# Kernel optimization log

Hardware: AMD Instinct MI355X
Metric: run time of the kernel (lower is better)

The kernel has to match this reference:

```python
import jax, jax.numpy as jnp
import numpy as np

N_EMB = 1024
EMB_DIM = 256
BETA = 0.25


def setup_inputs() -> dict:
    key = jax.random.key(0)
    k1, k2 = jax.random.split(key)
    z = jax.random.normal(k1, (32, EMB_DIM, 32, 32), dtype=jnp.float32)
    init = 1.0 / N_EMB
    emb = jax.random.uniform(k2, (N_EMB, EMB_DIM), dtype=jnp.float32,
                             minval=-init, maxval=init)
    return {"z": z, "emb": emb}


def reference(z, emb):
    # z: [B, C, H, W] -> [B, H, W, C]
    zc = jnp.transpose(z, (0, 2, 3, 1))
    z_flat = zc.reshape(-1, EMB_DIM)  # [N, D]

    # squared L2 distances: ||z||^2 + ||e||^2 - 2 z.e^T  -> [N, K]
    distances = (jnp.sum(z_flat ** 2, axis=1, keepdims=True)
                 + jnp.sum(emb ** 2, axis=1)
                 - 2.0 * (z_flat @ emb.T))
    nearest_idx = jnp.argmin(distances, axis=1)           # [N]
    nearest = jax.nn.one_hot(nearest_idx, N_EMB, dtype=jnp.float32)  # [N, K]

    # direct gather == one-hot matmul, same math
    zq = emb[nearest_idx].reshape(zc.shape)               # [B, H, W, C]

    loss = (jnp.mean((jax.lax.stop_gradient(zq) - zc) ** 2)
            + BETA * jnp.mean((zq - jax.lax.stop_gradient(zc)) ** 2))

    # straight-through estimator
    zq_st = zc + jax.lax.stop_gradient(zq - zc)

    e_mean = jnp.mean(nearest, axis=0)                    # [K]
    perplexity = jnp.exp(-jnp.sum(e_mean * jnp.log(e_mean + 1e-10)))

    zq_out = jnp.transpose(zq_st, (0, 3, 1, 2))           # back to NCHW
    return zq_out, loss, perplexity, nearest, nearest_idx[:, None]
```

## Files before the change

kernel.cpp:

```cpp
#include <hip/hip_runtime.h>

#define N_EMB  1024
#define EMB_D  256
#define HW     1024

#define OUT_ZQ      0
#define OUT_LOSS    8388608
#define OUT_PERP    8388609
#define OUT_NEAREST 8388610
#define OUT_IDX     41943042

#define WS_HIST   0
#define WS_ESQ    4096
#define WS_LOSSP  8192
#define WS_EH     12288
#define WS_TOTAL  536576

typedef unsigned long long ull;
typedef _Float16 half8 __attribute__((ext_vector_type(8)));
typedef float f32x4 __attribute__((ext_vector_type(4)));
typedef ull ull2 __attribute__((ext_vector_type(2)));

#define L_A     0
#define L_B     32768
#define L_ESQ   49152
#define L_ZSQ   53248
#define L_WIN   53504
#define L_RED   53760
#define L_TOT   55808

__device__ __forceinline__ void gload16(const void* g, void* l) {
    __builtin_amdgcn_global_load_lds(
        (const __attribute__((address_space(1))) unsigned int*)g,
        (__attribute__((address_space(3))) unsigned int*)l, 16, 0, 0);
}

__device__ __forceinline__ float pairwise8_combine(const float r[8]) {
    return __fadd_rn(__fadd_rn(__fadd_rn(r[0], r[1]), __fadd_rn(r[2], r[3])),
                     __fadd_rn(__fadd_rn(r[4], r[5]), __fadd_rn(r[6], r[7])));
}

__global__ void split_e(const float* __restrict__ emb, _Float16* __restrict__ eh) {
    int c = blockIdx.x;
    int k = threadIdx.x;
    eh[c * EMB_D + k] = (_Float16)emb[c * EMB_D + k];
}

__global__ void esq_kernel(const float* __restrict__ emb, float* __restrict__ esq,
                           int* __restrict__ hist) {
    int c = blockIdx.x * 256 + threadIdx.x;
    const float* p = emb + (size_t)c * EMB_D;
    float tot[2];
    #pragma unroll
    for (int h = 0; h < 2; ++h) {
        float r[8];
        #pragma unroll
        for (int i = 0; i < 8; ++i) {
            float x = p[h * 128 + i];
            r[i] = __fmul_rn(x, x);
        }
        for (int k = 8; k < 128; k += 8) {
            #pragma unroll
            for (int i = 0; i < 8; ++i) {
                float x = p[h * 128 + k + i];
                r[i] = __fadd_rn(r[i], __fmul_rn(x, x));
            }
        }
        tot[h] = pairwise8_combine(r);
    }
    esq[c] = __fadd_rn(tot[0], tot[1]);
    hist[c] = 0;
}

__global__ __launch_bounds__(256) void fused_vq(
        const float* __restrict__ z, const float* __restrict__ emb,
        const _Float16* __restrict__ eh, const float* __restrict__ esq,
        float* __restrict__ out, int* __restrict__ hist,
        double* __restrict__ lossp) {
    __shared__ __align__(16) char lds[L_TOT];
    int t = threadIdx.x, bid = blockIdx.x;
    int b = bid >> 4, hw0 = (bid & 15) << 6;
    int lane = t & 63, wave = t >> 6;
    int wm = wave >> 1, wn = wave & 1;
    int l15 = lane & 15, lq = lane >> 4;

    if (t >= 128) {
        int i = t - 128;
        #pragma unroll
        for (int q = 0; q < 8; ++q)
            *(float*)(lds + L_ESQ + (q * 128 + i) * 4) = esq[q * 128 + i];
    } else {
        int nl = t & 63, h = (t >> 6) & 1;
        const float* zp = z + ((size_t)b << 18) + hw0 + nl;
        int kb = h << 7;
        int abase = L_A + nl * 512;
        int sw = (nl & 7) << 4;
        float r[8];
        {   half8 hv;
            #pragma unroll
            for (int e = 0; e < 8; ++e) {
                float x = zp[(size_t)(kb + e) << 10];
                hv[e] = (_Float16)x;
                r[e] = __fmul_rn(x, x);
            }
            *(half8*)(lds + abase + (((kb << 1)) ^ sw)) = hv;
        }
        for (int c8 = 1; c8 < 16; ++c8) {
            half8 hv;
            #pragma unroll
            for (int e = 0; e < 8; ++e) {
                float x = zp[(size_t)(kb + c8 * 8 + e) << 10];
                hv[e] = (_Float16)x;
                r[e] = __fadd_rn(r[e], __fmul_rn(x, x));
            }
            *(half8*)(lds + abase + (((kb << 1) + c8 * 16) ^ sw)) = hv;
        }
        *(float*)(lds + L_RED + (h * 64 + nl) * 4) = pairwise8_combine(r);
    }
    __syncthreads();
    if (t < 64) {
        float t0 = *(float*)(lds + L_RED + t * 4);
        float t1 = *(float*)(lds + L_RED + 256 + t * 4);
        *(float*)(lds + L_ZSQ + t * 4) = __fadd_rn(t0, t1);
    }
    __syncthreads();

    int aoffs[2][2], boffs[4][2];
    #pragma unroll
    for (int i = 0; i < 2; ++i) {
        int r = wm * 32 + i * 16 + l15;
        #pragma unroll
        for (int kc = 0; kc < 2; ++kc)
            aoffs[i][kc] = L_A + r * 512 + ((kc * 64 + lq * 16) ^ ((r & 7) << 4));
    }
    #pragma unroll
    for (int j = 0; j < 4; ++j) {
        int c = wn * 64 + j * 16 + l15;
        #pragma unroll
        for (int kc = 0; kc < 2; ++kc)
            boffs[j][kc] = L_B + c * 128 + ((kc * 64 + lq * 16) ^ ((c & 7) << 4));
    }
    int bsrc[4], bdst[4];
    #pragma unroll
    for (int is = 0; is < 4; ++is) {
        int o = is * 4096 + t * 16;
        int col = o >> 7;
        int K = (o & 127) ^ ((col & 7) << 4);
        bsrc[is] = col * 256 + (K >> 1);
        bdst[is] = L_B + o;
    }
    float zs[8];
    #pragma unroll
    for (int s = 0; s < 8; ++s) {
        int row = wm * 32 + (s >> 2) * 16 + lq * 4 + (s & 3);
        zs[s] = *(const float*)(lds + L_ZSQ + row * 4);
    }
    ull k1[8], k2[8];
    #pragma unroll
    for (int s = 0; s < 8; ++s) { k1[s] = ~0ULL; k2[s] = ~0ULL; }

    for (int cbt = 0; cbt < 8; ++cbt) {
        f32x4 acc[2][4];
        #pragma unroll
        for (int i = 0; i < 2; ++i)
            #pragma unroll
            for (int j = 0; j < 4; ++j) acc[i][j] = (f32x4){0.f, 0.f, 0.f, 0.f};

        for (int kt = 0; kt < 4; ++kt) {
            __syncthreads();
            #pragma unroll
            for (int is = 0; is < 4; ++is)
                gload16(eh + cbt * 32768 + kt * 64 + bsrc[is], lds + bdst[is]);
            __syncthreads();

            half8 a[2][2], bb[4][2];
            #pragma unroll
            for (int i = 0; i < 2; ++i) {
                a[i][0] = *(const half8*)(lds + aoffs[i][0] + kt * 128);
                a[i][1] = *(const half8*)(lds + aoffs[i][1] + kt * 128);
            }
            #pragma unroll
            for (int j = 0; j < 4; ++j) {
                bb[j][0] = *(const half8*)(lds + boffs[j][0]);
                bb[j][1] = *(const half8*)(lds + boffs[j][1]);
            }
            #pragma unroll
            for (int i = 0; i < 2; ++i)
                #pragma unroll
                for (int j = 0; j < 4; ++j) {
                    acc[i][j] = __builtin_amdgcn_mfma_f32_16x16x32_f16(a[i][0], bb[j][0], acc[i][j], 0, 0, 0);
                    acc[i][j] = __builtin_amdgcn_mfma_f32_16x16x32_f16(a[i][1], bb[j][1], acc[i][j], 0, 0, 0);
                }
        }
        float es[4];
        #pragma unroll
        for (int j = 0; j < 4; ++j)
            es[j] = *(const float*)(lds + L_ESQ + ((cbt << 7) + wn * 64 + j * 16 + l15) * 4);
        #pragma unroll
        for (int i = 0; i < 2; ++i)
            #pragma unroll
            for (int r = 0; r < 4; ++r) {
                const int s = i * 4 + r;
                float zsv = zs[s];
                #pragma unroll
                for (int j = 0; j < 4; ++j) {
                    float d = __fsub_rn(__fadd_rn(zsv, es[j]), __fmul_rn(2.0f, acc[i][j][r]));
                    int cg = (cbt << 7) + wn * 64 + j * 16 + l15;
                    ull key = ((ull)__float_as_uint(d) << 32) | (unsigned)cg;
                    if (key < k1[s]) { k2[s] = k1[s]; k1[s] = key; }
                    else if (key < k2[s]) { k2[s] = key; }
                }
            }
    }

    __syncthreads();
    #pragma unroll
    for (int s = 0; s < 8; ++s) {
        int row = wm * 32 + (s >> 2) * 16 + lq * 4 + (s & 3);
        *(ull2*)(lds + L_A + row * 512 + ((wn << 4) + l15) * 16) = (ull2){k1[s], k2[s]};
    }
    __syncthreads();

    for (int rr = 0; rr < 16; ++rr) {
        int row = wave * 16 + rr;
        ull k = *(const ull*)(lds + L_A + row * 512 + lane * 8);
        ull kmin = k;
        #pragma unroll
        for (int m = 1; m < 64; m <<= 1) {
            ull o = __shfl_xor(kmin, m, 64);
            kmin = o < kmin ? o : kmin;
        }
        float dmin = __uint_as_float((unsigned)(kmin >> 32));
        float dme  = __uint_as_float((unsigned)(k >> 32));
        bool cand = dme <= __fadd_rn(dmin, 2e-4f);
        ull bal = __ballot(cand);
        int winner;
        if (__popcll(bal) == 1) {
            winner = (int)(unsigned)(kmin & 0xFFFFFFFFu);
        } else {
            const float* zp2 = z + ((size_t)b << 18) + hw0 + row;
            float zr[4];
            #pragma unroll
            for (int e = 0; e < 4; ++e) zr[e] = zp2[(size_t)(lane + 64 * e) << 10];
            float zsr = *(const float*)(lds + L_ZSQ + row * 4);
            ull bestk = ~0ULL;
            while (bal) {
                int src = __ffsll(bal) - 1;
                bal &= bal - 1;
                ull ck = __shfl(k, src, 64);
                int c = (int)(unsigned)(ck & 0xFFFFFFFFu);
                const float* ep = emb + (size_t)c * EMB_D;
                float p = __fmul_rn(zr[3], ep[lane + 192]);
                p = __builtin_fmaf(zr[2], ep[lane + 128], p);
                p = __builtin_fmaf(zr[1], ep[lane + 64], p);
                p = __builtin_fmaf(zr[0], ep[lane], p);
                #pragma unroll
                for (int m = 1; m < 64; m <<= 1)
                    p = __fadd_rn(p, __shfl_xor(p, m, 64));
                float ec = *(const float*)(lds + L_ESQ + c * 4);
                float d = __fsub_rn(__fadd_rn(zsr, ec), __fmul_rn(2.0f, p));
                ull kk = ((ull)__float_as_uint(d) << 32) | (unsigned)c;
                bestk = kk < bestk ? kk : bestk;
            }
            winner = (int)(unsigned)(bestk & 0xFFFFFFFFu);
        }
        size_t n = (size_t)bid * 64 + row;
        float* np = out + OUT_NEAREST + (n << 10);
        #pragma unroll
        for (int q = 0; q < 4; ++q) {
            int c4 = q * 256 + lane * 4;
            float4 v = { winner == c4     ? 1.f : 0.f, winner == c4 + 1 ? 1.f : 0.f,
                         winner == c4 + 2 ? 1.f : 0.f, winner == c4 + 3 ? 1.f : 0.f };
            *(float4*)(np + c4) = v;
        }
        if (lane == 0) {
            out[OUT_IDX + n] = (float)winner;
            atomicAdd(&hist[winner], 1);
            *(int*)(lds + L_WIN + row * 4) = winner;
        }
    }
    __syncthreads();

    {
        int hwl = t & 63, cq = t >> 6;
        int widx = *(const int*)(lds + L_WIN + hwl * 4);
        const float* zp3 = z + ((size_t)b << 18) + hw0 + hwl;
        float* oq = out + OUT_ZQ + ((size_t)b << 18) + hw0 + hwl;
        const float* er = emb + (size_t)widx * EMB_D;
        double s = 0.0;
        for (int cg = 0; cg < 16; ++cg) {
            int c0 = cq * 64 + cg * 4;
            float4 ev = *(const float4*)(er + c0);
            float evv[4] = {ev.x, ev.y, ev.z, ev.w};
            #pragma unroll
            for (int e = 0; e < 4; ++e) {
                size_t off = (size_t)(c0 + e) << 10;
                float zc = zp3[off];
                float diff = __fsub_rn(evv[e], zc);
                oq[off] = __fadd_rn(zc, diff);
                s += (double)__fmul_rn(diff, diff);
            }
        }
        *(double*)(lds + L_RED + t * 8) = s;
        __syncthreads();
        for (int st = 128; st > 0; st >>= 1) {
            if (t < st) {
                double o = *(double*)(lds + L_RED + (t + st) * 8);
                *(double*)(lds + L_RED + t * 8) += o;
            }
            __syncthreads();
        }
        if (t == 0) lossp[bid] = *(double*)(lds + L_RED);
    }
}

__global__ void finalize_scalars(const double* __restrict__ lossp,
                                 const int* __restrict__ hist,
                                 float* __restrict__ out_loss,
                                 float* __restrict__ out_perp) {
    __shared__ double sd[1024];
    int t = threadIdx.x;

    sd[t] = (t < 512) ? lossp[t] : 0.0;
    __syncthreads();
    for (int st = 512; st > 0; st >>= 1) {
        if (t < st) sd[t] += sd[t + st];
        __syncthreads();
    }
    if (t == 0) {
        double loss = 1.25 * (sd[0] / 8388608.0);
        *out_loss = (float)loss;
    }
    __syncthreads();

    float p = (float)hist[t] * (1.0f / 32768.0f);
    float term = __fmul_rn(p, logf(__fadd_rn(p, 1e-10f)));
    sd[t] = (double)term;
    __syncthreads();
    for (int st = 512; st > 0; st >>= 1) {
        if (t < st) sd[t] += sd[t + st];
        __syncthreads();
    }
    if (t == 0) *out_perp = expf(-(float)sd[0]);
}

extern "C" void kernel_launch(void* const* d_in, const int* in_sizes, int n_in,
                              void* d_out, int out_size, void* d_ws, size_t ws_size,
                              hipStream_t stream) {
    const float* z   = (const float*)d_in[0];
    const float* emb = (const float*)d_in[1];
    float* out = (float*)d_out;
    char*  ws  = (char*)d_ws;

    int*      hist  = (int*)(ws + WS_HIST);
    float*    esq   = (float*)(ws + WS_ESQ);
    double*   lossp = (double*)(ws + WS_LOSSP);
    _Float16* eh    = (_Float16*)(ws + WS_EH);

    esq_kernel<<<N_EMB / 256, 256, 0, stream>>>(emb, esq, hist);
    split_e<<<N_EMB, 256, 0, stream>>>(emb, eh);

    fused_vq<<<512, 256, 0, stream>>>(z, emb, eh, esq, out, hist, lossp);

    finalize_scalars<<<1, 1024, 0, stream>>>(lossp, hist,
                                             out + OUT_LOSS, out + OUT_PERP);
}
```

Measured before the change: 85.77 us.

## Double-buffer codebook tiles, merge prep kernels, fold finalize into last block

New measurement: 169.2 us. 1.97x slower.

```diff
diff --git a/kernel.cpp b/kernel.cpp
--- a/kernel.cpp
+++ b/kernel.cpp
@@ -13,8 +13,9 @@
 #define WS_HIST   0
 #define WS_ESQ    4096
 #define WS_LOSSP  8192
-#define WS_EH     12288
-#define WS_TOTAL  536576
+#define WS_CNT    12288
+#define WS_EH     16384
+#define WS_TOTAL  540672
 
 typedef unsigned long long ull;
 typedef _Float16 half8 __attribute__((ext_vector_type(8)));
@@ -23,11 +24,11 @@
 
 #define L_A     0
 #define L_B     32768
-#define L_ESQ   49152
-#define L_ZSQ   53248
-#define L_WIN   53504
-#define L_RED   53760
-#define L_TOT   55808
+#define L_ESQ   65536
+#define L_ZSQ   69632
+#define L_WIN   69888
+#define L_RED   70144
+#define L_TOT   72192
 
 __device__ __forceinline__ void gload16(const void* g, void* l) {
     __builtin_amdgcn_global_load_lds(
@@ -40,15 +41,16 @@
                      __fadd_rn(__fadd_rn(r[4], r[5]), __fadd_rn(r[6], r[7])));
 }
 
-__global__ void split_e(const float* __restrict__ emb, _Float16* __restrict__ eh) {
-    int c = blockIdx.x;
-    int k = threadIdx.x;
-    eh[c * EMB_D + k] = (_Float16)emb[c * EMB_D + k];
-}
-
-__global__ void esq_kernel(const float* __restrict__ emb, float* __restrict__ esq,
-                           int* __restrict__ hist) {
-    int c = blockIdx.x * 256 + threadIdx.x;
+__global__ void prep(const float* __restrict__ emb, _Float16* __restrict__ eh,
+                     float* __restrict__ esq, int* __restrict__ hist,
+                     unsigned* __restrict__ cnt) {
+    int bid = blockIdx.x;
+    if (bid < 1024) {
+        int c = bid, k = threadIdx.x;
+        eh[c * EMB_D + k] = (_Float16)emb[c * EMB_D + k];
+        return;
+    }
+    int c = (bid - 1024) * 256 + threadIdx.x;
     const float* p = emb + (size_t)c * EMB_D;
     float tot[2];
     #pragma unroll
@@ -70,25 +72,42 @@
     }
     esq[c] = __fadd_rn(tot[0], tot[1]);
     hist[c] = 0;
+    if (bid == 1024 && threadIdx.x == 0) *cnt = 0;
 }
 
 __global__ __launch_bounds__(256) void fused_vq(
         const float* __restrict__ z, const float* __restrict__ emb,
         const _Float16* __restrict__ eh, const float* __restrict__ esq,
         float* __restrict__ out, int* __restrict__ hist,
-        double* __restrict__ lossp) {
+        double* __restrict__ lossp, unsigned* __restrict__ cnt) {
     __shared__ __align__(16) char lds[L_TOT];
+    __shared__ unsigned lastflag;
     int t = threadIdx.x, bid = blockIdx.x;
     int b = bid >> 4, hw0 = (bid & 15) << 6;
     int lane = t & 63, wave = t >> 6;
     int wm = wave >> 1, wn = wave & 1;
     int l15 = lane & 15, lq = lane >> 4;
 
+    int bsrc[4], bdst[4];
+    #pragma unroll
+    for (int is = 0; is < 4; ++is) {
+        int o = is * 4096 + t * 16;
+        int col = o >> 7;
+        int K = (o & 127) ^ ((col & 7) << 4);
+        bsrc[is] = col * 256 + (K >> 1);
+        bdst[is] = L_B + o;
+    }
+    #pragma unroll
+    for (int is = 0; is < 4; ++is)
+        gload16(eh + bsrc[is], lds + bdst[is]);
+
     if (t >= 128) {
         int i = t - 128;
         #pragma unroll
-        for (int q = 0; q < 8; ++q)
-            *(float*)(lds + L_ESQ + (q * 128 + i) * 4) = esq[q * 128 + i];
+        for (int q = 0; q < 2; ++q) {
+            f32x4 v = *(const f32x4*)(esq + (q * 128 + i) * 4);
+            *(f32x4*)(lds + L_ESQ + (q * 128 + i) * 16) = v;
+        }
     } else {
         int nl = t & 63, h = (t >> 6) & 1;
         const float* zp = z + ((size_t)b << 18) + hw0 + nl;
@@ -140,15 +159,6 @@
         for (int kc = 0; kc < 2; ++kc)
             boffs[j][kc] = L_B + c * 128 + ((kc * 64 + lq * 16) ^ ((c & 7) << 4));
     }
-    int bsrc[4], bdst[4];
-    #pragma unroll
-    for (int is = 0; is < 4; ++is) {
-        int o = is * 4096 + t * 16;
-        int col = o >> 7;
-        int K = (o & 127) ^ ((col & 7) << 4);
-        bsrc[is] = col * 256 + (K >> 1);
-        bdst[is] = L_B + o;
-    }
     float zs[8];
     #pragma unroll
     for (int s = 0; s < 8; ++s) {
@@ -167,11 +177,9 @@
             for (int j = 0; j < 4; ++j) acc[i][j] = (f32x4){0.f, 0.f, 0.f, 0.f};
 
         for (int kt = 0; kt < 4; ++kt) {
+            const int r = cbt * 4 + kt;
             __syncthreads();
-            #pragma unroll
-            for (int is = 0; is < 4; ++is)
-                gload16(eh + cbt * 32768 + kt * 64 + bsrc[is], lds + bdst[is]);
-            __syncthreads();
+            const int cur = (r & 1) << 14;
 
             half8 a[2][2], bb[4][2];
             #pragma unroll
@@ -181,8 +189,16 @@
             }
             #pragma unroll
             for (int j = 0; j < 4; ++j) {
-                bb[j][0] = *(const half8*)(lds + boffs[j][0]);
-                bb[j][1] = *(const half8*)(lds + boffs[j][1]);
+                bb[j][0] = *(const half8*)(lds + boffs[j][0] + cur);
+                bb[j][1] = *(const half8*)(lds + boffs[j][1] + cur);
+            }
+            if (r < 31) {
+                const int rn = r + 1, cbn = rn >> 2, ktn = rn & 3;
+                const int nxt = (rn & 1) << 14;
+                #pragma unroll
+                for (int is = 0; is < 4; ++is)
+                    gload16(eh + cbn * 32768 + ktn * 64 + bsrc[is],
+                            lds + bdst[is] + nxt);
             }
             #pragma unroll
             for (int i = 0; i < 2; ++i)
@@ -269,9 +285,9 @@
         #pragma unroll
         for (int q = 0; q < 4; ++q) {
             int c4 = q * 256 + lane * 4;
-            float4 v = { winner == c4     ? 1.f : 0.f, winner == c4 + 1 ? 1.f : 0.f,
-                         winner == c4 + 2 ? 1.f : 0.f, winner == c4 + 3 ? 1.f : 0.f };
-            *(float4*)(np + c4) = v;
+            f32x4 v = { winner == c4     ? 1.f : 0.f, winner == c4 + 1 ? 1.f : 0.f,
+                        winner == c4 + 2 ? 1.f : 0.f, winner == c4 + 3 ? 1.f : 0.f };
+            __builtin_nontemporal_store(v, (f32x4*)(np + c4));
         }
         if (lane == 0) {
             out[OUT_IDX + n] = (float)winner;
@@ -282,24 +298,24 @@
     __syncthreads();
 
     {
-        int hwl = t & 63, cq = t >> 6;
-        int widx = *(const int*)(lds + L_WIN + hwl * 4);
-        const float* zp3 = z + ((size_t)b << 18) + hw0 + hwl;
-        float* oq = out + OUT_ZQ + ((size_t)b << 18) + hw0 + hwl;
-        const float* er = emb + (size_t)widx * EMB_D;
+        int q = t & 15;
+        int cq = t >> 4;
+        int4 w4 = *(const int4*)(lds + L_WIN + q * 16);
+        const float* zb = z + ((size_t)b << 18) + hw0 + q * 4;
+        float* ob = out + OUT_ZQ + ((size_t)b << 18) + hw0 + q * 4;
         double s = 0.0;
-        for (int cg = 0; cg < 16; ++cg) {
-            int c0 = cq * 64 + cg * 4;
-            float4 ev = *(const float4*)(er + c0);
-            float evv[4] = {ev.x, ev.y, ev.z, ev.w};
-            #pragma unroll
-            for (int e = 0; e < 4; ++e) {
-                size_t off = (size_t)(c0 + e) << 10;
-                float zc = zp3[off];
-                float diff = __fsub_rn(evv[e], zc);
-                oq[off] = __fadd_rn(zc, diff);
-                s += (double)__fmul_rn(diff, diff);
-            }
+        for (int i = 0; i < 16; ++i) {
+            int c = cq + (i << 4);
+            f32x4 zc = *(const f32x4*)(zb + ((size_t)c << 10));
+            f32x4 ev = { emb[(size_t)w4.x * EMB_D + c], emb[(size_t)w4.y * EMB_D + c],
+                         emb[(size_t)w4.z * EMB_D + c], emb[(size_t)w4.w * EMB_D + c] };
+            f32x4 df = { __fsub_rn(ev[0], zc[0]), __fsub_rn(ev[1], zc[1]),
+                         __fsub_rn(ev[2], zc[2]), __fsub_rn(ev[3], zc[3]) };
+            f32x4 st = { __fadd_rn(zc[0], df[0]), __fadd_rn(zc[1], df[1]),
+                         __fadd_rn(zc[2], df[2]), __fadd_rn(zc[3], df[3]) };
+            __builtin_nontemporal_store(st, (f32x4*)(ob + ((size_t)c << 10)));
+            s += (double)__fmul_rn(df[0], df[0]) + (double)__fmul_rn(df[1], df[1])
+               + (double)__fmul_rn(df[2], df[2]) + (double)__fmul_rn(df[3], df[3]);
         }
         *(double*)(lds + L_RED + t * 8) = s;
         __syncthreads();
@@ -312,36 +328,47 @@
         }
         if (t == 0) lossp[bid] = *(double*)(lds + L_RED);
     }
-}
-
-__global__ void finalize_scalars(const double* __restrict__ lossp,
-                                 const int* __restrict__ hist,
-                                 float* __restrict__ out_loss,
-                                 float* __restrict__ out_perp) {
-    __shared__ double sd[1024];
-    int t = threadIdx.x;
-
-    sd[t] = (t < 512) ? lossp[t] : 0.0;
-    __syncthreads();
-    for (int st = 512; st > 0; st >>= 1) {
-        if (t < st) sd[t] += sd[t + st];
+
+    __threadfence();
+    if (t == 0) lastflag = atomicAdd(cnt, 1u);
+    __syncthreads();
+    if (lastflag == 511u) {
+        volatile double* lp = lossp;
+        double s = lp[t] + lp[t + 256];
+        *(double*)(lds + L_RED + t * 8) = s;
         __syncthreads();
-    }
-    if (t == 0) {
-        double loss = 1.25 * (sd[0] / 8388608.0);
-        *out_loss = (float)loss;
-    }
-    __syncthreads();
-
-    float p = (float)hist[t] * (1.0f / 32768.0f);
-    float term = __fmul_rn(p, logf(__fadd_rn(p, 1e-10f)));
-    sd[t] = (double)term;
-    __syncthreads();
-    for (int st = 512; st > 0; st >>= 1) {
-        if (t < st) sd[t] += sd[t + st];
+        for (int st = 128; st > 0; st >>= 1) {
+            if (t < st) {
+                double o = *(double*)(lds + L_RED + (t + st) * 8);
+                *(double*)(lds + L_RED + t * 8) += o;
+            }
+            __syncthreads();
+        }
+        if (t == 0) {
+            double loss = 1.25 * ((*(double*)(lds + L_RED)) / 8388608.0);
+            out[OUT_LOSS] = (float)loss;
+        }
         __syncthreads();
-    }
-    if (t == 0) *out_perp = expf(-(float)sd[0]);
+
+        volatile int* hv = hist;
+        double ps = 0.0;
+        #pragma unroll
+        for (int qh = 0; qh < 4; ++qh) {
+            float p = (float)hv[t + qh * 256] * (1.0f / 32768.0f);
+            float term = __fmul_rn(p, logf(__fadd_rn(p, 1e-10f)));
+            ps += (double)term;
+        }
+        *(double*)(lds + L_RED + t * 8) = ps;
+        __syncthreads();
+        for (int st = 128; st > 0; st >>= 1) {
+            if (t < st) {
+                double o = *(double*)(lds + L_RED + (t + st) * 8);
+                *(double*)(lds + L_RED + t * 8) += o;
+            }
+            __syncthreads();
+        }
+        if (t == 0) out[OUT_PERP] = expf(-(float)(*(double*)(lds + L_RED)));
+    }
 }
 
 extern "C" void kernel_launch(void* const* d_in, const int* in_sizes, int n_in,
@@ -355,13 +382,9 @@
     int*      hist  = (int*)(ws + WS_HIST);
     float*    esq   = (float*)(ws + WS_ESQ);
     double*   lossp = (double*)(ws + WS_LOSSP);
+    unsigned* cnt   = (unsigned*)(ws + WS_CNT);
     _Float16* eh    = (_Float16*)(ws + WS_EH);
 
-    esq_kernel<<<N_EMB / 256, 256, 0, stream>>>(emb, esq, hist);
-    split_e<<<N_EMB, 256, 0, stream>>>(emb, eh);
-
-    fused_vq<<<512, 256, 0, stream>>>(z, emb, eh, esq, out, hist, lossp);
-
-    finalize_scalars<<<1, 1024, 0, stream>>>(lossp, hist,
-                                             out + OUT_LOSS, out + OUT_PERP);
-}
+    prep<<<1028, 256, 0, stream>>>(emb, eh, esq, hist, cnt);
+    fused_vq<<<512, 256, 0, stream>>>(z, emb, eh, esq, out, hist, lossp, cnt);
+}
```
